# Kernel tuning notes

Hardware: AMD Instinct MI355X
Metric: run time of the kernel (lower is better)

## Reference

```python
import jax, jax.numpy as jnp
import numpy as np

BITS = 4
GROUP_SIZE = 128
IN_F = 4096
OUT_F = 11008
MAXQ = (1 << BITS) - 1
PACK = 32 // BITS  # 8 values per int32 word


def setup_inputs() -> dict:
    key = jax.random.key(0)
    k1, k2, k3, k4, k5 = jax.random.split(key, 5)
    x = jax.random.normal(k1, (2, 2048, IN_F), dtype=jnp.float32)
    qweight = jax.random.randint(k2, (IN_F // PACK, OUT_F), 0, 2147483647, dtype=jnp.int32)
    qzeros = jax.random.randint(k3, (IN_F // GROUP_SIZE, OUT_F // PACK), 0, 2147483647, dtype=jnp.int32)
    scales = jax.random.uniform(k4, (IN_F // GROUP_SIZE, OUT_F), dtype=jnp.float32) * 0.01 + 1e-4
    bias = jax.random.normal(k5, (OUT_F,), dtype=jnp.float32)
    return {"x": x, "qweight": qweight, "qzeros": qzeros, "scales": scales, "bias": bias}


def _dequant_weight(qweight, qzeros, scales):
    shifts = jnp.arange(0, 32, BITS, dtype=jnp.int32)
    # unpack packed int4 weights: [K/8, N] -> [K/8, 8, N] -> [K, N]
    w = (qweight[:, None, :] >> shifts[None, :, None]) & MAXQ
    w = w.reshape(-1, qweight.shape[-1]).astype(jnp.float32)  # [K, N]
    # unpack zero points: [G, N/8] -> [G, N/8, 8] -> [G, N]
    z = (qzeros[:, :, None] >> shifts[None, None, :]) & MAXQ
    z = z.reshape(qzeros.shape[0], -1).astype(jnp.float32)  # [G, N]
    gidx = jnp.arange(w.shape[0]) // GROUP_SIZE  # [K]
    # asymmetric group-wise dequant: (q - zero) * scale
    return (w - z[gidx]) * scales[gidx].astype(jnp.float32)  # [K, N]


def reference(x, qweight, qzeros, scales, bias):
    raw_dtype = x.dtype
    W = _dequant_weight(qweight, qzeros, scales)  # [K, N] fp32
    x2 = x.astype(jnp.float32).reshape(-1, x.shape[-1])  # [M, K]
    out = x2 @ W + bias.astype(jnp.float32)  # [M, N]
    return out.astype(raw_dtype).reshape(x.shape[:-1] + (W.shape[-1],))
```

## Files before the change

kernel.cpp:

```cpp
#include <hip/hip_runtime.h>
#include <hip/hip_bf16.h>
#include <stdint.h>

#define K_DIM 4096
#define N_DIM 11008
#define GROUP 128

typedef __attribute__((ext_vector_type(8))) __bf16 bf16x8;
typedef __attribute__((ext_vector_type(4))) float f32x4;
typedef __attribute__((address_space(3))) uint8_t lds_u8;
typedef __attribute__((address_space(3))) void lds_void;
typedef __attribute__((address_space(1))) const void g_void;

static __device__ inline __bf16 f2bf(float f) { return (__bf16)f; }

__global__ __launch_bounds__(256) void cvt_x_kernel(const float* __restrict__ x,
                                                    __bf16* __restrict__ xb, int total8) {
    int t = blockIdx.x * 256 + threadIdx.x;
    if (t >= total8) return;
    f32x4 a0 = *(const f32x4*)(x + (size_t)t * 8);
    f32x4 a1 = *(const f32x4*)(x + (size_t)t * 8 + 4);
    bf16x8 v;
    #pragma unroll
    for (int j = 0; j < 4; ++j) { v[j] = f2bf(a0[j]); v[j + 4] = f2bf(a1[j]); }
    *(bf16x8*)(xb + (size_t)t * 8) = v;
}

__global__ __launch_bounds__(256) void dequant_w_kernel(const int* __restrict__ qw,
                                                        const int* __restrict__ qz,
                                                        const float* __restrict__ sc,
                                                        __bf16* __restrict__ wb) {
    const int n   = blockIdx.x * 256 + threadIdx.x;
    const int kb0 = blockIdx.y * 8;
    const int g   = blockIdx.y >> 1;
    const float s   = sc[(size_t)g * N_DIM + n];
    const float nzs = -(float)((qz[(size_t)g * (N_DIM / 8) + (n >> 3)] >> ((n & 7) * 4)) & 15) * s;
    #pragma unroll
    for (int j = 0; j < 8; ++j) {
        const int w = qw[(size_t)(kb0 + j) * N_DIM + n];
        bf16x8 v;
        #pragma unroll
        for (int b = 0; b < 8; ++b)
            v[b] = f2bf(fmaf((float)((w >> (4 * b)) & 15), s, nzs));
        *(bf16x8*)(wb + (size_t)n * K_DIM + (size_t)(kb0 + j) * 8) = v;
    }
}

#define BM2 256
#define BN2 256
#define BK2 64
#define NT  (K_DIM / BK2)

__global__ __launch_bounds__(512, 2) void gemm256_kernel(
    const __bf16* __restrict__ xb, const __bf16* __restrict__ wb,
    const float* __restrict__ bias, float* __restrict__ out)
{
    __shared__ __align__(16) __bf16 As[2][BM2 * BK2];
    __shared__ __align__(16) __bf16 Bs[2][BN2 * BK2];

    const int tid  = threadIdx.x;
    const int lane = tid & 63;
    const int wid  = tid >> 6;
    const int wm = (wid >> 2) * 128;
    const int wn = (wid & 3) * 64;

    const int bid = blockIdx.x;
    const int wg  = (bid & 7) * 86 + (bid >> 3);
    const int m0 = (wg / 43) * BM2;
    const int n0 = (wg % 43) * BN2;

    const __bf16* pa[4];
    const __bf16* pb[4];
    int chk[4];
    #pragma unroll
    for (int l = 0; l < 4; ++l) {
        const int ch  = l * 512 + tid;
        const int row = ch >> 3;
        const int g   = (ch & 7) ^ (row & 7);
        chk[l] = ch;
        pa[l] = xb + (size_t)(m0 + row) * K_DIM + g * 8;
        pb[l] = wb + (size_t)(n0 + row) * K_DIM + g * 8;
    }
    lds_u8* baseA = (lds_u8*)&As[0][0];
    lds_u8* baseB = (lds_u8*)&Bs[0][0];

    auto STAGE = [&](int buf, int kofs) {
        lds_u8* dA_ = baseA + buf * (BM2 * BK2 * 2);
        lds_u8* dB_ = baseB + buf * (BN2 * BK2 * 2);
        #pragma unroll
        for (int l = 0; l < 4; ++l)
            __builtin_amdgcn_global_load_lds((g_void*)(pa[l] + kofs),
                                             (lds_void*)(dA_ + chk[l] * 16), 16, 0, 0);
        #pragma unroll
        for (int l = 0; l < 4; ++l)
            __builtin_amdgcn_global_load_lds((g_void*)(pb[l] + kofs),
                                             (lds_void*)(dB_ + chk[l] * 16), 16, 0, 0);
    };

    const int fr  = lane & 15;
    const int fc  = lane >> 4;
    const int swz = fr & 7;
    const int col0 = (fc ^ swz) * 8;
    const int col1 = ((4 + fc) ^ swz) * 8;
    const int rowoffA = (wm + fr) * BK2;
    const int rowoffB = (wn + fr) * BK2;

    f32x4 acc[8][4];
    #pragma unroll
    for (int m = 0; m < 8; ++m)
        #pragma unroll
        for (int n = 0; n < 4; ++n) acc[m][n] = (f32x4){0.f, 0.f, 0.f, 0.f};

    STAGE(0, 0);
    STAGE(1, BK2);
    asm volatile("s_waitcnt vmcnt(8)" ::: "memory");
    __builtin_amdgcn_sched_barrier(0);
    __builtin_amdgcn_s_barrier();
    __builtin_amdgcn_sched_barrier(0);

    for (int t = 0; t < NT; ++t) {
        const int cur = t & 1;
        const __bf16* ra = &As[0][0] + cur * (BM2 * BK2) + rowoffA;
        const __bf16* rb = &Bs[0][0] + cur * (BN2 * BK2) + rowoffB;
        bf16x8 aR[8], bR[8], a2[8];

        #pragma unroll
        for (int n = 0; n < 2; ++n) {
            bR[n * 2 + 0] = *(const bf16x8*)(rb + n * 1024 + col0);
            bR[n * 2 + 1] = *(const bf16x8*)(rb + n * 1024 + col1);
        }
        #pragma unroll
        for (int m = 0; m < 4; ++m) {
            aR[m * 2 + 0] = *(const bf16x8*)(ra + m * 1024 + col0);
            aR[m * 2 + 1] = *(const bf16x8*)(ra + m * 1024 + col1);
        }
        __builtin_amdgcn_s_setprio(1);
        #pragma unroll
        for (int kk = 0; kk < 2; ++kk)
            #pragma unroll
            for (int m = 0; m < 4; ++m)
                #pragma unroll
                for (int n = 0; n < 2; ++n)
                    acc[m][n] = __builtin_amdgcn_mfma_f32_16x16x32_bf16(
                        aR[m * 2 + kk], bR[n * 2 + kk], acc[m][n], 0, 0, 0);
        __builtin_amdgcn_s_setprio(0);

        #pragma unroll
        for (int n = 2; n < 4; ++n) {
            bR[n * 2 + 0] = *(const bf16x8*)(rb + n * 1024 + col0);
            bR[n * 2 + 1] = *(const bf16x8*)(rb + n * 1024 + col1);
        }
        __builtin_amdgcn_s_setprio(1);
        #pragma unroll
        for (int kk = 0; kk < 2; ++kk)
            #pragma unroll
            for (int m = 0; m < 4; ++m)
                #pragma unroll
                for (int n = 2; n < 4; ++n)
                    acc[m][n] = __builtin_amdgcn_mfma_f32_16x16x32_bf16(
                        aR[m * 2 + kk], bR[n * 2 + kk], acc[m][n], 0, 0, 0);
        __builtin_amdgcn_s_setprio(0);

        #pragma unroll
        for (int m = 0; m < 4; ++m) {
            a2[m * 2 + 0] = *(const bf16x8*)(ra + (m + 4) * 1024 + col0);
            a2[m * 2 + 1] = *(const bf16x8*)(ra + (m + 4) * 1024 + col1);
        }
        asm volatile("s_waitcnt lgkmcnt(0)" ::: "memory");
        __builtin_amdgcn_sched_barrier(0);
        __builtin_amdgcn_s_barrier();
        __builtin_amdgcn_sched_barrier(0);
        if (t + 2 < NT) STAGE(cur, (t + 2) * BK2);

        __builtin_amdgcn_s_setprio(1);
        #pragma unroll
        for (int kk = 0; kk < 2; ++kk)
            #pragma unroll
            for (int m = 0; m < 4; ++m)
                #pragma unroll
                for (int n = 0; n < 4; ++n)
                    acc[m + 4][n] = __builtin_amdgcn_mfma_f32_16x16x32_bf16(
                        a2[m * 2 + kk], bR[n * 2 + kk], acc[m + 4][n], 0, 0, 0);
        __builtin_amdgcn_s_setprio(0);

        if (t + 2 < NT) { asm volatile("s_waitcnt vmcnt(8)" ::: "memory"); }
        else            { asm volatile("s_waitcnt vmcnt(0)" ::: "memory"); }
        __builtin_amdgcn_sched_barrier(0);
        __builtin_amdgcn_s_barrier();
        __builtin_amdgcn_sched_barrier(0);
    }

    const int cn  = lane & 15;
    const int cr4 = (lane >> 4) * 4;
    #pragma unroll
    for (int n = 0; n < 4; ++n) {
        const int col = n0 + wn + n * 16 + cn;
        const float bv = bias[col];
        #pragma unroll
        for (int m = 0; m < 8; ++m) {
            const int row = m0 + wm + m * 16 + cr4;
            #pragma unroll
            for (int r = 0; r < 4; ++r)
                out[(size_t)(row + r) * N_DIM + col] = acc[m][n][r] + bv;
        }
    }
}

#define FBM 128
#define FBN 128
#define FBK 32
#define FLDSS 40
__global__ __launch_bounds__(256) void gptq_gemm_fused_kernel(
    const float* __restrict__ x, const int* __restrict__ qw, const int* __restrict__ qz,
    const float* __restrict__ sc, const float* __restrict__ bias, float* __restrict__ out)
{
    __shared__ __align__(16) __bf16 Asm[FBM][FLDSS];
    __shared__ __align__(16) __bf16 Bsm[FBN][FLDSS];
    const int tid = threadIdx.x, lane = tid & 63, wid = tid >> 6;
    const int m0 = blockIdx.y * FBM, n0 = blockIdx.x * FBN;
    const int wm = (wid >> 1) * 64, wn = (wid & 1) * 64;
    f32x4 acc[4][4];
    #pragma unroll
    for (int i = 0; i < 4; ++i)
        #pragma unroll
        for (int j = 0; j < 4; ++j) acc[i][j] = (f32x4){0.f, 0.f, 0.f, 0.f};
    const int a_m = tid >> 2, a_h = tid & 3;
    const int b_n = tid & 127, b_k8 = tid >> 7;
    const int ng = n0 + b_n, zsh = (ng & 7) * 4;
    const int fr = lane & 15, fc = lane >> 4;
    for (int k0 = 0; k0 < K_DIM; k0 += FBK) {
        const int g = k0 >> 7;
        const float* xa = x + (size_t)(m0 + a_m) * K_DIM + k0 + a_h * 8;
        f32x4 a0 = *(const f32x4*)xa;
        f32x4 a1 = *(const f32x4*)(xa + 4);
        const float* xbp = xa + (size_t)64 * K_DIM;
        f32x4 a2 = *(const f32x4*)xbp;
        f32x4 a3 = *(const f32x4*)(xbp + 4);
        const int kb = (k0 >> 3) + b_k8;
        const int w0 = qw[(size_t)kb * N_DIM + ng];
        const int w1 = qw[(size_t)(kb + 2) * N_DIM + ng];
        const float s = sc[(size_t)g * N_DIM + ng];
        const float nzs = -(float)((qz[(size_t)g * (N_DIM / 8) + (ng >> 3)] >> zsh) & 15) * s;
        __syncthreads();
        bf16x8 av0, av1;
        #pragma unroll
        for (int j = 0; j < 4; ++j) {
            av0[j] = f2bf(a0[j]); av0[j + 4] = f2bf(a1[j]);
            av1[j] = f2bf(a2[j]); av1[j + 4] = f2bf(a3[j]);
        }
        *(bf16x8*)&Asm[a_m][a_h * 8] = av0;
        *(bf16x8*)&Asm[a_m + 64][a_h * 8] = av1;
        bf16x8 bv0, bv1;
        #pragma unroll
        for (int j = 0; j < 8; ++j) {
            bv0[j] = f2bf(fmaf((float)((w0 >> (4 * j)) & 15), s, nzs));
            bv1[j] = f2bf(fmaf((float)((w1 >> (4 * j)) & 15), s, nzs));
        }
        *(bf16x8*)&Bsm[b_n][b_k8 * 8] = bv0;
        *(bf16x8*)&Bsm[b_n][(b_k8 + 2) * 8] = bv1;
        __syncthreads();
        bf16x8 af[4], bfr[4];
        #pragma unroll
        for (int i = 0; i < 4; ++i) af[i] = *(const bf16x8*)&Asm[wm + i * 16 + fr][fc * 8];
        #pragma unroll
        for (int j = 0; j < 4; ++j) bfr[j] = *(const bf16x8*)&Bsm[wn + j * 16 + fr][fc * 8];
        #pragma unroll
        for (int i = 0; i < 4; ++i)
            #pragma unroll
            for (int j = 0; j < 4; ++j)
                acc[i][j] = __builtin_amdgcn_mfma_f32_16x16x32_bf16(af[i], bfr[j], acc[i][j], 0, 0, 0);
    }
    const int cn = lane & 15, cr4 = (lane >> 4) * 4;
    #pragma unroll
    for (int j = 0; j < 4; ++j) {
        const int col = n0 + wn + j * 16 + cn;
        const float bv = bias[col];
        #pragma unroll
        for (int i = 0; i < 4; ++i) {
            const int row = m0 + wm + i * 16 + cr4;
            #pragma unroll
            for (int r = 0; r < 4; ++r)
                out[(size_t)(row + r) * N_DIM + col] = acc[i][j][r] + bv;
        }
    }
}

extern "C" void kernel_launch(void* const* d_in, const int* in_sizes, int n_in,
                              void* d_out, int out_size, void* d_ws, size_t ws_size,
                              hipStream_t stream) {
    const float* x    = (const float*)d_in[0];
    const int*   qw   = (const int*)d_in[1];
    const int*   qz   = (const int*)d_in[2];
    const float* sc   = (const float*)d_in[3];
    const float* bias = (const float*)d_in[4];
    float* out = (float*)d_out;
    const int M = in_sizes[0] / K_DIM;

    const size_t xb_bytes = (size_t)M * K_DIM * sizeof(__bf16);
    const size_t wb_bytes = (size_t)N_DIM * K_DIM * sizeof(__bf16);
    if (ws_size >= xb_bytes + wb_bytes && (M % BM2) == 0) {
        __bf16* xb = (__bf16*)d_ws;
        __bf16* wb = (__bf16*)((uint8_t*)d_ws + xb_bytes);
        const int total8 = M * K_DIM / 8;
        cvt_x_kernel<<<dim3(total8 / 256), dim3(256), 0, stream>>>(x, xb, total8);
        dequant_w_kernel<<<dim3(N_DIM / 256, K_DIM / 8 / 8), dim3(256), 0, stream>>>(qw, qz, sc, wb);
        const int nblocks = (N_DIM / BN2) * (M / BM2);
        gemm256_kernel<<<dim3(nblocks), dim3(512), 0, stream>>>(xb, wb, bias, out);
    } else {
        gptq_gemm_fused_kernel<<<dim3(N_DIM / FBN, M / FBM), dim3(256), 0, stream>>>(x, qw, qz, sc, bias, out);
    }
}
```

Measured before the change: 417.3 us.

## Use 4 waves with 128x128 warp tiles in the bf16 GEMM

The GEMM block shrinks from 8 waves to 4 waves, each computing a 128x128 output tile (8x8 MFMA accumulators) instead of 128x64. Each thread now issues 8 global-to-LDS loads per operand per stage, and the wait counts are adjusted to match. The B fragments are loaded in one batch and the MFMA loop order is changed. The aim is to raise register-level reuse of LDS fragments, at the cost of much higher VGPR/AGPR pressure (256 accumulator floats per lane), one block per CU, and fewer waves available to hide latency.

```diff
diff --git a/kernel.cpp b/kernel.cpp
--- a/kernel.cpp
+++ b/kernel.cpp
@@ -51,7 +51,7 @@
 #define BK2 64
 #define NT  (K_DIM / BK2)
 
-__global__ __launch_bounds__(512, 2) void gemm256_kernel(
+__global__ __launch_bounds__(256, 1) void gemm_w128_kernel(
     const __bf16* __restrict__ xb, const __bf16* __restrict__ wb,
     const float* __restrict__ bias, float* __restrict__ out)
 {
@@ -61,40 +61,31 @@
     const int tid  = threadIdx.x;
     const int lane = tid & 63;
     const int wid  = tid >> 6;
-    const int wm = (wid >> 2) * 128;
-    const int wn = (wid & 3) * 64;
+    const int wm = (wid >> 1) * 128;
+    const int wn = (wid & 1) * 128;
 
     const int bid = blockIdx.x;
     const int wg  = (bid & 7) * 86 + (bid >> 3);
     const int m0 = (wg / 43) * BM2;
     const int n0 = (wg % 43) * BN2;
 
-    const __bf16* pa[4];
-    const __bf16* pb[4];
-    int chk[4];
-    #pragma unroll
-    for (int l = 0; l < 4; ++l) {
-        const int ch  = l * 512 + tid;
-        const int row = ch >> 3;
-        const int g   = (ch & 7) ^ (row & 7);
-        chk[l] = ch;
-        pa[l] = xb + (size_t)(m0 + row) * K_DIM + g * 8;
-        pb[l] = wb + (size_t)(n0 + row) * K_DIM + g * 8;
-    }
+    const int gsw = (tid & 7) ^ ((tid >> 3) & 7);
+    const __bf16* pa_base = xb + (size_t)(m0 + (tid >> 3)) * K_DIM + gsw * 8;
+    const __bf16* pb_base = wb + (size_t)(n0 + (tid >> 3)) * K_DIM + gsw * 8;
     lds_u8* baseA = (lds_u8*)&As[0][0];
     lds_u8* baseB = (lds_u8*)&Bs[0][0];
 
     auto STAGE = [&](int buf, int kofs) {
-        lds_u8* dA_ = baseA + buf * (BM2 * BK2 * 2);
-        lds_u8* dB_ = baseB + buf * (BN2 * BK2 * 2);
-        #pragma unroll
-        for (int l = 0; l < 4; ++l)
-            __builtin_amdgcn_global_load_lds((g_void*)(pa[l] + kofs),
-                                             (lds_void*)(dA_ + chk[l] * 16), 16, 0, 0);
-        #pragma unroll
-        for (int l = 0; l < 4; ++l)
-            __builtin_amdgcn_global_load_lds((g_void*)(pb[l] + kofs),
-                                             (lds_void*)(dB_ + chk[l] * 16), 16, 0, 0);
+        lds_u8* dA_ = baseA + buf * (BM2 * BK2 * 2) + tid * 16;
+        lds_u8* dB_ = baseB + buf * (BN2 * BK2 * 2) + tid * 16;
+        #pragma unroll
+        for (int l = 0; l < 8; ++l)
+            __builtin_amdgcn_global_load_lds((g_void*)(pa_base + kofs + (size_t)l * 32 * K_DIM),
+                                             (lds_void*)(dA_ + l * 4096), 16, 0, 0);
+        #pragma unroll
+        for (int l = 0; l < 8; ++l)
+            __builtin_amdgcn_global_load_lds((g_void*)(pb_base + kofs + (size_t)l * 32 * K_DIM),
+                                             (lds_void*)(dB_ + l * 4096), 16, 0, 0);
     };
 
     const int fr  = lane & 15;
@@ -105,15 +96,15 @@
     const int rowoffA = (wm + fr) * BK2;
     const int rowoffB = (wn + fr) * BK2;
 
-    f32x4 acc[8][4];
+    f32x4 acc[8][8];
     #pragma unroll
     for (int m = 0; m < 8; ++m)
         #pragma unroll
-        for (int n = 0; n < 4; ++n) acc[m][n] = (f32x4){0.f, 0.f, 0.f, 0.f};
+        for (int n = 0; n < 8; ++n) acc[m][n] = (f32x4){0.f, 0.f, 0.f, 0.f};
 
     STAGE(0, 0);
     STAGE(1, BK2);
-    asm volatile("s_waitcnt vmcnt(8)" ::: "memory");
+    asm volatile("s_waitcnt vmcnt(16)" ::: "memory");
     __builtin_amdgcn_sched_barrier(0);
     __builtin_amdgcn_s_barrier();
     __builtin_amdgcn_sched_barrier(0);
@@ -122,10 +113,10 @@
         const int cur = t & 1;
         const __bf16* ra = &As[0][0] + cur * (BM2 * BK2) + rowoffA;
         const __bf16* rb = &Bs[0][0] + cur * (BN2 * BK2) + rowoffB;
-        bf16x8 aR[8], bR[8], a2[8];
-
-        #pragma unroll
-        for (int n = 0; n < 2; ++n) {
+        bf16x8 aR[8], bR[16], a2[8];
+
+        #pragma unroll
+        for (int n = 0; n < 8; ++n) {
             bR[n * 2 + 0] = *(const bf16x8*)(rb + n * 1024 + col0);
             bR[n * 2 + 1] = *(const bf16x8*)(rb + n * 1024 + col1);
         }
@@ -136,32 +127,16 @@
         }
         __builtin_amdgcn_s_setprio(1);
         #pragma unroll
-        for (int kk = 0; kk < 2; ++kk)
-            #pragma unroll
-            for (int m = 0; m < 4; ++m)
+        for (int m = 0; m < 4; ++m)
+            #pragma unroll
+            for (int n = 0; n < 8; ++n)
                 #pragma unroll
-                for (int n = 0; n < 2; ++n)
+                for (int kk = 0; kk < 2; ++kk)
                     acc[m][n] = __builtin_amdgcn_mfma_f32_16x16x32_bf16(
                         aR[m * 2 + kk], bR[n * 2 + kk], acc[m][n], 0, 0, 0);
         __builtin_amdgcn_s_setprio(0);
 
         #pragma unroll
-        for (int n = 2; n < 4; ++n) {
-            bR[n * 2 + 0] = *(const bf16x8*)(rb + n * 1024 + col0);
-            bR[n * 2 + 1] = *(const bf16x8*)(rb + n * 1024 + col1);
-        }
-        __builtin_amdgcn_s_setprio(1);
-        #pragma unroll
-        for (int kk = 0; kk < 2; ++kk)
-            #pragma unroll
-            for (int m = 0; m < 4; ++m)
-                #pragma unroll
-                for (int n = 2; n < 4; ++n)
-                    acc[m][n] = __builtin_amdgcn_mfma_f32_16x16x32_bf16(
-                        aR[m * 2 + kk], bR[n * 2 + kk], acc[m][n], 0, 0, 0);
-        __builtin_amdgcn_s_setprio(0);
-
-        #pragma unroll
         for (int m = 0; m < 4; ++m) {
             a2[m * 2 + 0] = *(const bf16x8*)(ra + (m + 4) * 1024 + col0);
             a2[m * 2 + 1] = *(const bf16x8*)(ra + (m + 4) * 1024 + col1);
@@ -174,17 +149,17 @@
 
         __builtin_amdgcn_s_setprio(1);
         #pragma unroll
-        for (int kk = 0; kk < 2; ++kk)
-            #pragma unroll
-            for (int m = 0; m < 4; ++m)
+        for (int m = 0; m < 4; ++m)
+            #pragma unroll
+            for (int n = 0; n < 8; ++n)
                 #pragma unroll
-                for (int n = 0; n < 4; ++n)
+                for (int kk = 0; kk < 2; ++kk)
                     acc[m + 4][n] = __builtin_amdgcn_mfma_f32_16x16x32_bf16(
                         a2[m * 2 + kk], bR[n * 2 + kk], acc[m + 4][n], 0, 0, 0);
         __builtin_amdgcn_s_setprio(0);
 
-        if (t + 2 < NT) { asm volatile("s_waitcnt vmcnt(8)" ::: "memory"); }
-        else            { asm volatile("s_waitcnt vmcnt(0)" ::: "memory"); }
+        if (t + 2 < NT) { asm volatile("s_waitcnt vmcnt(16)" ::: "memory"); }
+        else            { asm volatile("s_waitcnt vmcnt(0)"  ::: "memory"); }
         __builtin_amdgcn_sched_barrier(0);
         __builtin_amdgcn_s_barrier();
         __builtin_amdgcn_sched_barrier(0);
@@ -193,7 +168,7 @@
     const int cn  = lane & 15;
     const int cr4 = (lane >> 4) * 4;
     #pragma unroll
-    for (int n = 0; n < 4; ++n) {
+    for (int n = 0; n < 8; ++n) {
         const int col = n0 + wn + n * 16 + cn;
         const float bv = bias[col];
         #pragma unroll
@@ -305,7 +280,7 @@
         cvt_x_kernel<<<dim3(total8 / 256), dim3(256), 0, stream>>>(x, xb, total8);
         dequant_w_kernel<<<dim3(N_DIM / 256, K_DIM / 8 / 8), dim3(256), 0, stream>>>(qw, qz, sc, wb);
         const int nblocks = (N_DIM / BN2) * (M / BM2);
-        gemm256_kernel<<<dim3(nblocks), dim3(512), 0, stream>>>(xb, wb, bias, out);
+        gemm_w128_kernel<<<dim3(nblocks), dim3(256), 0, stream>>>(xb, wb, bias, out);
     } else {
         gptq_gemm_fused_kernel<<<dim3(N_DIM / FBN, M / FBM), dim3(256), 0, stream>>>(x, qw, qz, sc, bias, out);
     }
```

After: 615.0 us. +47.4%, slower.
